# Performance work log

Measured on AMD Instinct MI355X. Metric: run time of the kernel, lower is better.

Reference implementation:

```python
import jax, jax.numpy as jnp
import numpy as np
import math

H = 1024      # hidden_size
NH = 16       # num_heads
HD = H // NH  # head_dim
MS = 256      # memory_size
MD = 512      # memory_dim
B, S = 2, 2048


def setup_inputs() -> dict:
    key = jax.random.key(0)
    ks = jax.random.split(key, 12)
    sd = 1.0 / math.sqrt(H)
    inp = {
        "hidden_states": jax.random.normal(ks[0], (B, S, H), dtype=jnp.float32),
        "attention_mask": jnp.zeros((B, S), dtype=jnp.float32),
        "Wq": jax.random.normal(ks[1], (H, H), dtype=jnp.float32) * sd,
        "bq": jnp.zeros((H,), dtype=jnp.float32),
        "Wk": jax.random.normal(ks[2], (H, H), dtype=jnp.float32) * sd,
        "bk": jnp.zeros((H,), dtype=jnp.float32),
        "Wv": jax.random.normal(ks[3], (H, H), dtype=jnp.float32) * sd,
        "bv": jnp.zeros((H,), dtype=jnp.float32),
        "Wo": jax.random.normal(ks[4], (H, H), dtype=jnp.float32) * sd,
        "bo": jnp.zeros((H,), dtype=jnp.float32),
        "memory_values": jax.random.normal(ks[5], (MS, MD), dtype=jnp.float32),
        "Wmp": jax.random.normal(ks[6], (H, MD), dtype=jnp.float32) * (1.0 / math.sqrt(MD)),
        "bmp": jnp.zeros((H,), dtype=jnp.float32),
        "Wma": jax.random.normal(ks[7], (MS, H), dtype=jnp.float32) * sd,
        "bma": jnp.zeros((MS,), dtype=jnp.float32),
    }
    return inp


def reference(hidden_states, attention_mask, Wq, bq, Wk, bk, Wv, bv, Wo, bo,
              memory_values, Wmp, bmp, Wma, bma):
    b, s, h = hidden_states.shape
    scale = math.sqrt(HD)
    # projections (nn.Linear: x @ W.T + b)
    q = hidden_states @ Wq.T + bq
    k = hidden_states @ Wk.T + bk
    v = hidden_states @ Wv.T + bv
    # [b, nh, s, hd]
    q = q.reshape(b, s, NH, HD).transpose(0, 2, 1, 3)
    k = k.reshape(b, s, NH, HD).transpose(0, 2, 1, 3)
    v = v.reshape(b, s, NH, HD).transpose(0, 2, 1, 3)
    # full score matrix [b, nh, s, s] (faithful to original naive MHA)
    attn_scores = jnp.einsum('bhqd,bhkd->bhqk', q, k) / scale
    attn_scores = attn_scores + attention_mask[:, None, None, :] * (-1e9)
    attn_probs = jax.nn.softmax(attn_scores, axis=-1)  # dropout = identity (eval)
    attn_output = jnp.einsum('bhqk,bhkd->bhqd', attn_probs, v)
    attn_output = attn_output.transpose(0, 2, 1, 3).reshape(b, s, h)
    # memory-bank cross attention
    mem_scores = hidden_states @ Wma.T + bma            # [b, s, MS]
    mem_probs = jax.nn.softmax(mem_scores, axis=-1)
    mem_out = mem_probs @ memory_values                  # [b, s, MD]
    mem_out = mem_out @ Wmp.T + bmp                      # [b, s, H]
    combined = attn_output + 0.3 * mem_out
    return combined @ Wo.T + bo
```

## Files before the change

### kernel.cpp

```cpp
#include <hip/hip_runtime.h>

typedef __bf16 bf16;
typedef __bf16 bf16x8 __attribute__((ext_vector_type(8)));
typedef __bf16 bf16x4 __attribute__((ext_vector_type(4)));
typedef float  f32x4  __attribute__((ext_vector_type(4)));
typedef float  f32x16 __attribute__((ext_vector_type(16)));
typedef unsigned u32x2 __attribute__((ext_vector_type(2)));
typedef unsigned u32x4 __attribute__((ext_vector_type(4)));
typedef unsigned long long uptr;

#define MFMA16(a, b, c) __builtin_amdgcn_mfma_f32_16x16x32_bf16((a), (b), (c), 0, 0, 0)
#define MFMA32(a, b, c) __builtin_amdgcn_mfma_f32_32x32x16_bf16((a), (b), (c), 0, 0, 0)

__device__ __forceinline__ void gl_lds16(const void* g, void* l) {
  __builtin_amdgcn_global_load_lds(
      (__attribute__((address_space(1))) void*)(uptr)(g),
      (__attribute__((address_space(3))) void*)(uptr)(l),
      16, 0, 0);
}
__device__ __forceinline__ void gl_lds4(const void* g, void* l) {
  __builtin_amdgcn_global_load_lds(
      (__attribute__((address_space(1))) void*)(uptr)(g),
      (__attribute__((address_space(3))) void*)(uptr)(l),
      4, 0, 0);
}
__device__ __forceinline__ unsigned cvtpk_bf16(float lo, float hi) {
  unsigned r;
  asm("v_cvt_pk_bf16_f32 %0, %1, %2" : "=v"(r) : "v"(lo), "v"(hi));
  return r;
}

__global__ __launch_bounds__(256) void fused_prep(
    const float* __restrict__ X, const float* __restrict__ Wq,
    const float* __restrict__ Wk, const float* __restrict__ Wv,
    const float* __restrict__ Wo, const float* __restrict__ Wma,
    const float* __restrict__ Wmp, const float* __restrict__ mask,
    const float* __restrict__ bq, const float* __restrict__ bk,
    const float* __restrict__ bv, const float* __restrict__ mv,
    bf16* __restrict__ Xb, bf16* __restrict__ Wqkvb, bf16* __restrict__ Wob,
    bf16* __restrict__ Wmab, bf16* __restrict__ Wmpb,
    float* __restrict__ M2, float* __restrict__ bqkv, bf16* __restrict__ mvTb) {
  const int bid = blockIdx.x, t = threadIdx.x;
  const float QS = 0.125f * 1.44269504f;
  auto cvt = [&](const float* src, bf16* dst, int blk, float sc) {
    const long i = ((long)blk * 256 + t) * 4;
    const float4 v = *(const float4*)(src + i);
    bf16x4 o = {(bf16)(v.x * sc), (bf16)(v.y * sc), (bf16)(v.z * sc), (bf16)(v.w * sc)};
    *(bf16x4*)(dst + i) = o;
  };
  if (bid < 4096) cvt(X, Xb, bid, 1.0f);
  else if (bid < 5120) cvt(Wq, Wqkvb, bid - 4096, QS);
  else if (bid < 6144) cvt(Wk, Wqkvb + 1024 * 1024, bid - 5120, 1.0f);
  else if (bid < 7168) cvt(Wv, Wqkvb + 2 * 1024 * 1024, bid - 6144, 1.0f);
  else if (bid < 8192) cvt(Wo, Wob, bid - 7168, 1.0f);
  else if (bid < 8448) cvt(Wma, Wmab, bid - 8192, 1.0f);
  else if (bid < 8960) cvt(Wmp, Wmpb, bid - 8448, 1.0f);
  else if (bid < 8964) {
    const long i = ((long)(bid - 8960) * 256 + t) * 4;
    const float4 v = *(const float4*)(mask + i);
    float4 o = {v.x * -1.44269504e9f - 40.0f, v.y * -1.44269504e9f - 40.0f,
                v.z * -1.44269504e9f - 40.0f, v.w * -1.44269504e9f - 40.0f};
    *(float4*)(M2 + i) = o;
  } else if (bid < 8967) {
    const int s = bid - 8964;
    const float* src = s == 0 ? bq : (s == 1 ? bk : bv);
    const float sc = s == 0 ? QS : 1.0f;
    float4 v = *(const float4*)(src + t * 4);
    float4 o = {v.x * sc, v.y * sc, v.z * sc, v.w * sc};
    *(float4*)(bqkv + s * 1024 + t * 4) = o;
  } else {
    const int d = bid - 8967;
    mvTb[(long)d * 256 + t] = (bf16)mv[(long)t * 512 + d];
  }
}

__global__ __launch_bounds__(256) void softmax_rows256(const float* __restrict__ in,
                                                       bf16* __restrict__ out) {
  const int w = threadIdx.x >> 6, l = threadIdx.x & 63;
  const long row = (long)blockIdx.x * 4 + w;
  const float4 v = *(const float4*)(in + row * 256 + l * 4);
  float mx = fmaxf(fmaxf(v.x, v.y), fmaxf(v.z, v.w));
  mx = fmaxf(mx, __shfl_xor(mx, 1, 64));
  mx = fmaxf(mx, __shfl_xor(mx, 2, 64));
  mx = fmaxf(mx, __shfl_xor(mx, 4, 64));
  mx = fmaxf(mx, __shfl_xor(mx, 8, 64));
  mx = fmaxf(mx, __shfl_xor(mx, 16, 64));
  mx = fmaxf(mx, __shfl_xor(mx, 32, 64));
  const float e0 = __expf(v.x - mx), e1 = __expf(v.y - mx);
  const float e2 = __expf(v.z - mx), e3 = __expf(v.w - mx);
  float sm = e0 + e1 + e2 + e3;
  sm += __shfl_xor(sm, 1, 64);
  sm += __shfl_xor(sm, 2, 64);
  sm += __shfl_xor(sm, 4, 64);
  sm += __shfl_xor(sm, 8, 64);
  sm += __shfl_xor(sm, 16, 64);
  sm += __shfl_xor(sm, 32, 64);
  const float inv = 1.0f / sm;
  bf16x4 o = {(bf16)(e0 * inv), (bf16)(e1 * inv), (bf16)(e2 * inv), (bf16)(e3 * inv)};
  *(bf16x4*)(out + row * 256 + l * 4) = o;
}

template <typename OutT, bool HAS_ADD>
__global__ __launch_bounds__(256, 3) void gemm_bt(
    const bf16* __restrict__ A, const bf16* __restrict__ B,
    const float* __restrict__ bias, const bf16* __restrict__ addsrc,
    OutT* __restrict__ C, int M, int N, int K, float alpha) {
  __shared__ bf16 lA[2][128 * 64];
  __shared__ bf16 lB[2][64 * 64];
  const int tid = threadIdx.x;
  const int w = tid >> 6, l = tid & 63;
  const int hi = l >> 4, lo = l & 15;
  const int m0 = blockIdx.y * 128, n0 = blockIdx.x * 64;
  const int wm = w * 32;

  const int sr8 = l >> 3;
  const int sc = (l & 7) * 8;
  const long aRow = (long)(m0 + wm + sr8);
  const long bRow = (long)(n0 + w * 16 + sr8);

  auto stage = [&](int p, int k0) {
#pragma unroll
    for (int j = 0; j < 4; ++j)
      gl_lds16(A + (aRow + 8 * j) * K + k0 + sc, (char*)lA[p] + (wm + 8 * j) * 128);
#pragma unroll
    for (int j = 0; j < 2; ++j)
      gl_lds16(B + (bRow + 8 * j) * K + k0 + sc, (char*)lB[p] + (w * 16 + 8 * j) * 128);
  };

  f32x4 acc[2][4] = {};
  stage(0, 0);
  __syncthreads();
  const int nt = K >> 6;

  for (int t = 0; t < nt; ++t) {
    const int p = t & 1;
    if (t + 1 < nt) stage(p ^ 1, (t + 1) << 6);
#pragma unroll
    for (int kk = 0; kk < 2; ++kk) {
      bf16x8 af[2], bfr[4];
#pragma unroll
      for (int mi = 0; mi < 2; ++mi)
        af[mi] = *(const bf16x8*)((const char*)lA[p] + (wm + mi * 16 + lo) * 128 + kk * 64 + hi * 16);
#pragma unroll
      for (int ni = 0; ni < 4; ++ni)
        bfr[ni] = *(const bf16x8*)((const char*)lB[p] + (ni * 16 + lo) * 128 + kk * 64 + hi * 16);
      __builtin_amdgcn_s_setprio(1);
#pragma unroll
      for (int mi = 0; mi < 2; ++mi)
#pragma unroll
        for (int ni = 0; ni < 4; ++ni)
          acc[mi][ni] = MFMA16(af[mi], bfr[ni], acc[mi][ni]);
      __builtin_amdgcn_s_setprio(0);
    }
    __syncthreads();
  }

#pragma unroll
  for (int ni = 0; ni < 4; ++ni) {
    const int col = n0 + ni * 16 + lo;
    const float bv = bias ? bias[col] : 0.0f;
#pragma unroll
    for (int mi = 0; mi < 2; ++mi) {
      const int mrow = m0 + wm + mi * 16 + hi * 4;
#pragma unroll
      for (int r = 0; r < 4; ++r) {
        const long row = mrow + r;
        float v = (acc[mi][ni][r] + bv) * alpha;
        if (HAS_ADD) v += (float)addsrc[row * N + col];
        C[row * (long)N + col] = (OutT)v;
      }
    }
  }
}

__global__ __launch_bounds__(256, 3) void gemm_qkv(
    const bf16* __restrict__ A, const bf16* __restrict__ B,
    const float* __restrict__ bias, bf16* __restrict__ Qo,
    bf16* __restrict__ Ko, bf16* __restrict__ Vto) {
  const int K = 1024;
  __shared__ bf16 smem[2][128 * 64];
  bf16* lA = smem[0];
  bf16* lB = smem[1];
  const int tid = threadIdx.x;
  const int w = tid >> 6, l = tid & 63;
  const int hi = l >> 4, lo = l & 15;
  const int m0 = blockIdx.y * 128, n0 = blockIdx.x * 128;
  const int wm = (w >> 1) * 64, wn = (w & 1) * 64;

  const int sr = w * 32 + (l >> 3);
  const int sc = (l & 7) * 8;
  const long aBase = (long)(m0 + sr) * K + sc;
  const long bBase = (long)(n0 + sr) * K + sc;

  f32x4 acc[4][4] = {};

  for (int k0 = 0; k0 < K; k0 += 64) {
#pragma unroll
    for (int j = 0; j < 4; ++j) {
      gl_lds16(A + aBase + (long)8 * j * K + k0, (char*)lA + (w * 32 + 8 * j) * 128);
      gl_lds16(B + bBase + (long)8 * j * K + k0, (char*)lB + (w * 32 + 8 * j) * 128);
    }
    __syncthreads();
#pragma unroll
    for (int kk = 0; kk < 2; ++kk) {
      bf16x8 af[4], bfr[4];
#pragma unroll
      for (int i = 0; i < 4; ++i) {
        af[i]  = *(const bf16x8*)((const char*)lA + (wm + i * 16 + lo) * 128 + kk * 64 + hi * 16);
        bfr[i] = *(const bf16x8*)((const char*)lB + (wn + i * 16 + lo) * 128 + kk * 64 + hi * 16);
      }
#pragma unroll
      for (int mi = 0; mi < 4; ++mi)
#pragma unroll
        for (int ni = 0; ni < 4; ++ni)
          acc[mi][ni] = MFMA16(af[mi], bfr[ni], acc[mi][ni]);
    }
    __syncthreads();
  }

  const int region = n0 >> 10;
  if (region < 2) {
#pragma unroll
    for (int ni = 0; ni < 4; ++ni) {
      const int col = n0 + wn + ni * 16 + lo;
      const float bv = bias[col];
#pragma unroll
      for (int mi = 0; mi < 4; ++mi) {
        const int mrow = m0 + wm + mi * 16 + hi * 4;
#pragma unroll
        for (int r = 0; r < 4; ++r) {
          const long row = mrow + r;
          const float v = acc[mi][ni][r] + bv;
          if (region == 0) Qo[row * 1024 + col] = (bf16)v;
          else             Ko[row * 1024 + (col - 1024)] = (bf16)v;
        }
      }
    }
  } else {
    bf16* sT = smem[0];
#pragma unroll
    for (int ni = 0; ni < 4; ++ni) {
      const int cT = wn + ni * 16 + lo;
      const float bv = bias[n0 + cT];
#pragma unroll
      for (int mi = 0; mi < 4; ++mi) {
        const int rT = wm + mi * 16 + hi * 4;
        u32x2 pw = {cvtpk_bf16(acc[mi][ni][0] + bv, acc[mi][ni][1] + bv),
                    cvtpk_bf16(acc[mi][ni][2] + bv, acc[mi][ni][3] + bv)};
        *(u32x2*)((char*)sT + cT * 256 + ((rT * 2) ^ ((cT & 15) << 3))) = pw;
      }
    }
    __syncthreads();
    const long vrow0 = (long)(m0 >> 11) * 1024 + (n0 - 2048);
    const int srow = m0 & 2047;
#pragma unroll
    for (int dd = 0; dd < 32; ++dd) {
      const int d = w * 32 + dd;
      const unsigned pv = *(const unsigned*)((const char*)sT + d * 256 + ((l * 4) ^ ((d & 15) << 3)));
      *(unsigned*)((char*)(Vto + (vrow0 + d) * 2048 + srow) + l * 4) = pv;
    }
  }
}

__global__ __launch_bounds__(256, 4) void attn_fwd(
    const bf16* __restrict__ Q, const bf16* __restrict__ Km,
    const bf16* __restrict__ Vt, const float* __restrict__ M2,
    bf16* __restrict__ Opart, float* __restrict__ ml) {
  __shared__ bf16 lK[2][64 * 64];
  __shared__ bf16 lV[2][64 * 64];
  __shared__ alignas(16) float lM[2][64];
  const int tid = threadIdx.x, w = tid >> 6, l = tid & 63;
  const int q31 = l & 31, h32 = l >> 5;
  const int b = blockIdx.z >> 1, half = blockIdx.z & 1;
  const int hh = blockIdx.y, q0 = blockIdx.x * 128;
  const long S = 2048, H = 1024;
  const int kbase = half * 1024;

  bf16x8 qf[4];
  const long qrow = (long)b * S + q0 + w * 32 + q31;
#pragma unroll
  for (int sl = 0; sl < 4; ++sl)
    qf[sl] = *(const bf16x8*)(Q + qrow * H + hh * 64 + sl * 16 + h32 * 8);

  f32x16 o0 = {}, o1 = {};
  float lrun = 0.0f;

  const int swr = w * 16 + (l >> 3);
  const int swc = ((l & 7) ^ (l >> 3)) * 8;

  auto stage = [&](int p, int k0) {
#pragma unroll
    for (int j = 0; j < 2; ++j) {
      gl_lds16(Km + ((long)b * S + k0 + swr + 8 * j) * H + hh * 64 + swc,
               (char*)lK[p] + (w * 16 + 8 * j) * 128);
      gl_lds16(Vt + ((long)b * H + hh * 64 + swr + 8 * j) * S + k0 + swc,
               (char*)lV[p] + (w * 16 + 8 * j) * 128);
    }
    if (w == 0) gl_lds4(M2 + (long)b * S + k0 + l, (char*)lM[p]);
  };

  stage(0, kbase);
  __syncthreads();

  for (int t = 0; t < 16; ++t) {
    const int p = t & 1;
    if (t < 15) stage(p ^ 1, kbase + (t + 1) * 64);

    f32x16 s0, s1;
#pragma unroll
    for (int g = 0; g < 4; ++g) {
      const f32x4 m0 = *(const f32x4*)&lM[p][8 * g + 4 * h32];
      const f32x4 m1 = *(const f32x4*)&lM[p][32 + 8 * g + 4 * h32];
#pragma unroll
      for (int r = 0; r < 4; ++r) {
        s0[4 * g + r] = m0[r];
        s1[4 * g + r] = m1[r];
      }
    }

    __builtin_amdgcn_s_setprio(1);
#pragma unroll
    for (int sl = 0; sl < 4; ++sl) {
      const int ch = sl * 2 + h32;
      const int cx = (ch ^ (q31 & 7)) * 16;
      const bf16x8 k0f = *(const bf16x8*)((const char*)lK[p] + q31 * 128 + cx);
      const bf16x8 k1f = *(const bf16x8*)((const char*)lK[p] + (32 + q31) * 128 + cx);
      s0 = MFMA32(k0f, qf[sl], s0);
      s1 = MFMA32(k1f, qf[sl], s1);
    }
    __builtin_amdgcn_s_setprio(0);

#pragma unroll
    for (int i = 0; i < 16; ++i) s0[i] = __builtin_amdgcn_exp2f(s0[i]);
#pragma unroll
    for (int i = 0; i < 16; ++i) s1[i] = __builtin_amdgcn_exp2f(s1[i]);

    f32x16 ts;
#pragma unroll
    for (int i = 0; i < 16; ++i) ts[i] = s0[i] + s1[i];
#pragma unroll
    for (int i = 0; i < 8; ++i) ts[i] += ts[i + 8];
#pragma unroll
    for (int i = 0; i < 4; ++i) ts[i] += ts[i + 4];
    float rs = (ts[0] + ts[1]) + (ts[2] + ts[3]);
    rs += __shfl_xor(rs, 32, 64);
    lrun += rs;

    bf16x8 pa[4];
#pragma unroll
    for (int ks = 0; ks < 4; ++ks) {
      const int rb = (ks & 1) * 8;
      unsigned a0, a1, b0, b1;
      if (ks < 2) {
        a0 = cvtpk_bf16(s0[rb + 0], s0[rb + 1]);
        a1 = cvtpk_bf16(s0[rb + 2], s0[rb + 3]);
        b0 = cvtpk_bf16(s0[rb + 4], s0[rb + 5]);
        b1 = cvtpk_bf16(s0[rb + 6], s0[rb + 7]);
      } else {
        a0 = cvtpk_bf16(s1[rb + 0], s1[rb + 1]);
        a1 = cvtpk_bf16(s1[rb + 2], s1[rb + 3]);
        b0 = cvtpk_bf16(s1[rb + 4], s1[rb + 5]);
        b1 = cvtpk_bf16(s1[rb + 6], s1[rb + 7]);
      }
      const u32x2 r02 = __builtin_amdgcn_permlane32_swap(a0, b0, false, false);
      const u32x2 r13 = __builtin_amdgcn_permlane32_swap(a1, b1, false, false);
      const u32x4 pw = {r02[0], r13[0], r02[1], r13[1]};
      pa[ks] = __builtin_bit_cast(bf16x8, pw);
    }

    __builtin_amdgcn_s_setprio(1);
#pragma unroll
    for (int ks = 0; ks < 4; ++ks) {
      const int ch = ks * 2 + h32;
      const int cx = (ch ^ (q31 & 7)) * 16;
      const bf16x8 v0 = *(const bf16x8*)((const char*)lV[p] + q31 * 128 + cx);
      const bf16x8 v1 = *(const bf16x8*)((const char*)lV[p] + (32 + q31) * 128 + cx);
      o0 = MFMA32(pa[ks], v0, o0);
      o1 = MFMA32(pa[ks], v1, o1);
    }
    __builtin_amdgcn_s_setprio(0);
    __syncthreads();
  }

  if (h32 == 0)
    ml[((long)half * 4096 + (long)b * 2048 + q0 + w * 32 + q31) * 16 + hh] = lrun;
#pragma unroll
  for (int reg = 0; reg < 16; ++reg) {
    const int row = (reg & 3) + 8 * (reg >> 2) + 4 * h32;
    const long qg = (long)b * 2048 + q0 + w * 32 + row;
    Opart[((long)half * 4096 + qg) * 1024 + hh * 64 + q31]      = (bf16)o0[reg];
    Opart[((long)half * 4096 + qg) * 1024 + hh * 64 + 32 + q31] = (bf16)o1[reg];
  }
}

__global__ __launch_bounds__(256) void attn_combine(
    const bf16* __restrict__ Opart, const float* __restrict__ ml,
    bf16* __restrict__ AO) {
  const long i = ((long)blockIdx.x * 256 + threadIdx.x) * 4;
  const long qg = i >> 10;
  const int h = (int)((i & 1023) >> 6);
  const float l0 = ml[qg * 16 + h];
  const float l1 = ml[(4096 + qg) * 16 + h];
  const float inv = 1.0f / (l0 + l1);
  const bf16x4 O0 = *(const bf16x4*)(Opart + i);
  const bf16x4 O1 = *(const bf16x4*)(Opart + 4096L * 1024 + i);
  bf16x4 o;
#pragma unroll
  for (int j = 0; j < 4; ++j)
    o[j] = (bf16)(((float)O0[j] + (float)O1[j]) * inv);
  *(bf16x4*)(AO + i) = o;
}

extern "C" void kernel_launch(void* const* d_in, const int* in_sizes, int n_in,
                              void* d_out, int out_size, void* d_ws, size_t ws_size,
                              hipStream_t stream) {
  const float* X    = (const float*)d_in[0];
  const float* mask = (const float*)d_in[1];
  const float* Wq   = (const float*)d_in[2];  const float* bq  = (const float*)d_in[3];
  const float* Wk   = (const float*)d_in[4];  const float* bk  = (const float*)d_in[5];
  const float* Wv   = (const float*)d_in[6];  const float* bv  = (const float*)d_in[7];
  const float* Wo   = (const float*)d_in[8];  const float* bo  = (const float*)d_in[9];
  const float* mv   = (const float*)d_in[10];
  const float* Wmp  = (const float*)d_in[11]; const float* bmp = (const float*)d_in[12];
  const float* Wma  = (const float*)d_in[13]; const float* bma = (const float*)d_in[14];

  char* ws = (char*)d_ws;
  size_t off = 0;
  auto alloc = [&](size_t bytes) -> void* {
    void* p = ws + off;
    off += (bytes + 255) & ~(size_t)255;
    return p;
  };
  const long MS_ = 4096;
  bf16* Xb    = (bf16*)alloc(MS_ * 1024 * 2);
  bf16* Wqkvb = (bf16*)alloc(3072L * 1024 * 2);
  bf16* Wob   = (bf16*)alloc(1024 * 1024 * 2);
  bf16* Wmab  = (bf16*)alloc(256 * 1024 * 2);
  bf16* Wmpb  = (bf16*)alloc(1024 * 512 * 2);
  bf16* mvTb  = (bf16*)alloc(512 * 256 * 2);
  float* M2   = (float*)alloc(MS_ * 4);
  float* bqkv = (float*)alloc(3072 * 4);
  bf16* Qb    = (bf16*)alloc(MS_ * 1024 * 2);
  bf16* Kb    = (bf16*)alloc(MS_ * 1024 * 2);
  bf16* Vtb   = (bf16*)alloc(MS_ * 1024 * 2);
  bf16* AO    = (bf16*)alloc(MS_ * 1024 * 2);
  char* region = (char*)alloc(2 * MS_ * 1024 * 2 + MS_ * 16 * 8 + 1024);
  bf16* Opart = (bf16*)region;
  float* ml   = (float*)(region + 2 * MS_ * 1024 * 2);
  float* MSc  = (float*)region;
  bf16* MP    = (bf16*)(region + MS_ * 256 * 4);
  bf16* MO    = Kb;
  bf16* CB    = Qb;

  fused_prep<<<9479, 256, 0, stream>>>(X, Wq, Wk, Wv, Wo, Wma, Wmp, mask,
                                       bq, bk, bv, mv,
                                       Xb, Wqkvb, Wob, Wmab, Wmpb, M2, bqkv, mvTb);
  gemm_qkv<<<dim3(24, 32), 256, 0, stream>>>(Xb, Wqkvb, bqkv, Qb, Kb, Vtb);
  attn_fwd<<<dim3(16, 16, 4), 256, 0, stream>>>(Qb, Kb, Vtb, M2, Opart, ml);
  attn_combine<<<4096, 256, 0, stream>>>(Opart, ml, AO);
  gemm_bt<float, false><<<dim3(4, 32), 256, 0, stream>>>(Xb, Wmab, bma, nullptr, MSc, 4096, 256, 1024, 1.0f);
  softmax_rows256<<<1024, 256, 0, stream>>>(MSc, MP);
  gemm_bt<bf16, false><<<dim3(8, 32), 256, 0, stream>>>(MP, mvTb, nullptr, nullptr, MO, 4096, 512, 256, 1.0f);
  gemm_bt<bf16, true><<<dim3(16, 32), 256, 0, stream>>>(MO, Wmpb, bmp, AO, CB, 4096, 1024, 512, 0.3f);
  gemm_bt<float, false><<<dim3(16, 32), 256, 0, stream>>>(CB, Wob, bo, nullptr, (float*)d_out, 4096, 1024, 1024, 1.0f);
}
```

Measured before the change: 148.4 us.

## Fuse memory-score GEMM into QKV GEMM and attention combine into Wmp epilogue

Appends the Wma weights and bias to the concatenated QKV weight matrix, so the QKV GEMM grid grows by two column tiles and also writes the fp32 memory scores. This removes the separate memory-score GEMM launch. It also drops the attn_combine kernel and merges the two split-K attention partials inside the Wmp GEMM epilogue, which removes an extra pass over the AO buffer. The trade-off is a heavier epilogue with scattered ml/Opart loads and a per-element divide, plus separate workspace buffers instead of aliased ones.

```diff
diff --git a/kernel.cpp b/kernel.cpp
--- a/kernel.cpp
+++ b/kernel.cpp
@@ -36,9 +36,10 @@
     const float* __restrict__ Wo, const float* __restrict__ Wma,
     const float* __restrict__ Wmp, const float* __restrict__ mask,
     const float* __restrict__ bq, const float* __restrict__ bk,
-    const float* __restrict__ bv, const float* __restrict__ mv,
+    const float* __restrict__ bv, const float* __restrict__ bma,
+    const float* __restrict__ mv,
     bf16* __restrict__ Xb, bf16* __restrict__ Wqkvb, bf16* __restrict__ Wob,
-    bf16* __restrict__ Wmab, bf16* __restrict__ Wmpb,
+    bf16* __restrict__ Wmpb,
     float* __restrict__ M2, float* __restrict__ bqkv, bf16* __restrict__ mvTb) {
   const int bid = blockIdx.x, t = threadIdx.x;
   const float QS = 0.125f * 1.44269504f;
@@ -53,7 +54,7 @@
   else if (bid < 6144) cvt(Wk, Wqkvb + 1024 * 1024, bid - 5120, 1.0f);
   else if (bid < 7168) cvt(Wv, Wqkvb + 2 * 1024 * 1024, bid - 6144, 1.0f);
   else if (bid < 8192) cvt(Wo, Wob, bid - 7168, 1.0f);
-  else if (bid < 8448) cvt(Wma, Wmab, bid - 8192, 1.0f);
+  else if (bid < 8448) cvt(Wma, Wqkvb + 3072 * 1024, bid - 8192, 1.0f);
   else if (bid < 8960) cvt(Wmp, Wmpb, bid - 8448, 1.0f);
   else if (bid < 8964) {
     const long i = ((long)(bid - 8960) * 256 + t) * 4;
@@ -68,8 +69,10 @@
     float4 v = *(const float4*)(src + t * 4);
     float4 o = {v.x * sc, v.y * sc, v.z * sc, v.w * sc};
     *(float4*)(bqkv + s * 1024 + t * 4) = o;
+  } else if (bid < 8968) {
+    if (t < 64) *(float4*)(bqkv + 3072 + t * 4) = *(const float4*)(bma + t * 4);
   } else {
-    const int d = bid - 8967;
+    const int d = bid - 8968;
     mvTb[(long)d * 256 + t] = (bf16)mv[(long)t * 512 + d];
   }
 }
@@ -100,11 +103,12 @@
   *(bf16x4*)(out + row * 256 + l * 4) = o;
 }
 
-template <typename OutT, bool HAS_ADD>
+template <typename OutT, bool COMBINE>
 __global__ __launch_bounds__(256, 3) void gemm_bt(
     const bf16* __restrict__ A, const bf16* __restrict__ B,
-    const float* __restrict__ bias, const bf16* __restrict__ addsrc,
-    OutT* __restrict__ C, int M, int N, int K, float alpha) {
+    const float* __restrict__ bias, const bf16* __restrict__ Op,
+    const float* __restrict__ mlp, OutT* __restrict__ C,
+    int M, int N, int K, float alpha) {
   __shared__ bf16 lA[2][128 * 64];
   __shared__ bf16 lB[2][64 * 64];
   const int tid = threadIdx.x;
@@ -166,7 +170,14 @@
       for (int r = 0; r < 4; ++r) {
         const long row = mrow + r;
         float v = (acc[mi][ni][r] + bv) * alpha;
-        if (HAS_ADD) v += (float)addsrc[row * N + col];
+        if (COMBINE) {
+          const int h = col >> 6;
+          const float l0 = mlp[row * 16 + h];
+          const float l1 = mlp[(4096L + row) * 16 + h];
+          const float o0v = (float)Op[row * 1024 + col];
+          const float o1v = (float)Op[4096L * 1024 + row * 1024 + col];
+          v += (o0v + o1v) / (l0 + l1);
+        }
         C[row * (long)N + col] = (OutT)v;
       }
     }
@@ -176,7 +187,7 @@
 __global__ __launch_bounds__(256, 3) void gemm_qkv(
     const bf16* __restrict__ A, const bf16* __restrict__ B,
     const float* __restrict__ bias, bf16* __restrict__ Qo,
-    bf16* __restrict__ Ko, bf16* __restrict__ Vto) {
+    bf16* __restrict__ Ko, bf16* __restrict__ Vto, float* __restrict__ MSc) {
   const int K = 1024;
   __shared__ bf16 smem[2][128 * 64];
   bf16* lA = smem[0];
@@ -218,8 +229,7 @@
     __syncthreads();
   }
 
-  const int region = n0 >> 10;
-  if (region < 2) {
+  if (n0 < 2048) {
 #pragma unroll
     for (int ni = 0; ni < 4; ++ni) {
       const int col = n0 + wn + ni * 16 + lo;
@@ -231,12 +241,12 @@
         for (int r = 0; r < 4; ++r) {
           const long row = mrow + r;
           const float v = acc[mi][ni][r] + bv;
-          if (region == 0) Qo[row * 1024 + col] = (bf16)v;
-          else             Ko[row * 1024 + (col - 1024)] = (bf16)v;
+          if (n0 < 1024) Qo[row * 1024 + col] = (bf16)v;
+          else           Ko[row * 1024 + (col - 1024)] = (bf16)v;
         }
       }
     }
-  } else {
+  } else if (n0 < 3072) {
     bf16* sT = smem[0];
 #pragma unroll
     for (int ni = 0; ni < 4; ++ni) {
@@ -258,6 +268,20 @@
       const int d = w * 32 + dd;
       const unsigned pv = *(const unsigned*)((const char*)sT + d * 256 + ((l * 4) ^ ((d & 15) << 3)));
       *(unsigned*)((char*)(Vto + (vrow0 + d) * 2048 + srow) + l * 4) = pv;
+    }
+  } else {
+#pragma unroll
+    for (int ni = 0; ni < 4; ++ni) {
+      const int col = n0 + wn + ni * 16 + lo;
+      const float bv = bias[col];
+      const int cm = col - 3072;
+#pragma unroll
+      for (int mi = 0; mi < 4; ++mi) {
+        const int mrow = m0 + wm + mi * 16 + hi * 4;
+#pragma unroll
+        for (int r = 0; r < 4; ++r)
+          MSc[(long)(mrow + r) * 256 + cm] = acc[mi][ni][r] + bv;
+      }
     }
   }
 }
@@ -393,24 +417,6 @@
   }
 }
 
-__global__ __launch_bounds__(256) void attn_combine(
-    const bf16* __restrict__ Opart, const float* __restrict__ ml,
-    bf16* __restrict__ AO) {
-  const long i = ((long)blockIdx.x * 256 + threadIdx.x) * 4;
-  const long qg = i >> 10;
-  const int h = (int)((i & 1023) >> 6);
-  const float l0 = ml[qg * 16 + h];
-  const float l1 = ml[(4096 + qg) * 16 + h];
-  const float inv = 1.0f / (l0 + l1);
-  const bf16x4 O0 = *(const bf16x4*)(Opart + i);
-  const bf16x4 O1 = *(const bf16x4*)(Opart + 4096L * 1024 + i);
-  bf16x4 o;
-#pragma unroll
-  for (int j = 0; j < 4; ++j)
-    o[j] = (bf16)(((float)O0[j] + (float)O1[j]) * inv);
-  *(bf16x4*)(AO + i) = o;
-}
-
 extern "C" void kernel_launch(void* const* d_in, const int* in_sizes, int n_in,
                               void* d_out, int out_size, void* d_ws, size_t ws_size,
                               hipStream_t stream) {
@@ -433,34 +439,32 @@
   };
   const long MS_ = 4096;
   bf16* Xb    = (bf16*)alloc(MS_ * 1024 * 2);
-  bf16* Wqkvb = (bf16*)alloc(3072L * 1024 * 2);
+  bf16* Wqkvb = (bf16*)alloc(3328L * 1024 * 2);
   bf16* Wob   = (bf16*)alloc(1024 * 1024 * 2);
-  bf16* Wmab  = (bf16*)alloc(256 * 1024 * 2);
   bf16* Wmpb  = (bf16*)alloc(1024 * 512 * 2);
   bf16* mvTb  = (bf16*)alloc(512 * 256 * 2);
   float* M2   = (float*)alloc(MS_ * 4);
-  float* bqkv = (float*)alloc(3072 * 4);
+  float* bqkv = (float*)alloc(3328 * 4);
   bf16* Qb    = (bf16*)alloc(MS_ * 1024 * 2);
   bf16* Kb    = (bf16*)alloc(MS_ * 1024 * 2);
   bf16* Vtb   = (bf16*)alloc(MS_ * 1024 * 2);
-  bf16* AO    = (bf16*)alloc(MS_ * 1024 * 2);
-  char* region = (char*)alloc(2 * MS_ * 1024 * 2 + MS_ * 16 * 8 + 1024);
-  bf16* Opart = (bf16*)region;
-  float* ml   = (float*)(region + 2 * MS_ * 1024 * 2);
-  float* MSc  = (float*)region;
-  bf16* MP    = (bf16*)(region + MS_ * 256 * 4);
+  bf16* Opart = (bf16*)alloc(2 * MS_ * 1024 * 2);
+  float* ml   = (float*)alloc(2 * MS_ * 16 * 4);
+  float* MSc  = (float*)alloc(MS_ * 256 * 4);
+  bf16* MP    = (bf16*)alloc(MS_ * 256 * 2);
   bf16* MO    = Kb;
   bf16* CB    = Qb;
 
-  fused_prep<<<9479, 256, 0, stream>>>(X, Wq, Wk, Wv, Wo, Wma, Wmp, mask,
-                                       bq, bk, bv, mv,
-                                       Xb, Wqkvb, Wob, Wmab, Wmpb, M2, bqkv, mvTb);
-  gemm_qkv<<<dim3(24, 32), 256, 0, stream>>>(Xb, Wqkvb, bqkv, Qb, Kb, Vtb);
+  fused_prep<<<9480, 256, 0, stream>>>(X, Wq, Wk, Wv, Wo, Wma, Wmp, mask,
+                                       bq, bk, bv, bma, mv,
+                                       Xb, Wqkvb, Wob, Wmpb, M2, bqkv, mvTb);
+  gemm_qkv<<<dim3(26, 32), 256, 0, stream>>>(Xb, Wqkvb, bqkv, Qb, Kb, Vtb, MSc);
   attn_fwd<<<dim3(16, 16, 4), 256, 0, stream>>>(Qb, Kb, Vtb, M2, Opart, ml);
-  attn_combine<<<4096, 256, 0, stream>>>(Opart, ml, AO);
-  gemm_bt<float, false><<<dim3(4, 32), 256, 0, stream>>>(Xb, Wmab, bma, nullptr, MSc, 4096, 256, 1024, 1.0f);
   softmax_rows256<<<1024, 256, 0, stream>>>(MSc, MP);
-  gemm_bt<bf16, false><<<dim3(8, 32), 256, 0, stream>>>(MP, mvTb, nullptr, nullptr, MO, 4096, 512, 256, 1.0f);
-  gemm_bt<bf16, true><<<dim3(16, 32), 256, 0, stream>>>(MO, Wmpb, bmp, AO, CB, 4096, 1024, 512, 0.3f);
-  gemm_bt<float, false><<<dim3(16, 32), 256, 0, stream>>>(CB, Wob, bo, nullptr, (float*)d_out, 4096, 1024, 1024, 1.0f);
-}
+  gemm_bt<bf16, false><<<dim3(8, 32), 256, 0, stream>>>(MP, mvTb, nullptr, nullptr, nullptr,
+                                                        MO, 4096, 512, 256, 1.0f);
+  gemm_bt<bf16, true><<<dim3(16, 32), 256, 0, stream>>>(MO, Wmpb, bmp, Opart, ml,
+                                                        CB, 4096, 1024, 512, 0.3f);
+  gemm_bt<float, false><<<dim3(16, 32), 256, 0, stream>>>(CB, Wob, bo, nullptr, nullptr,
+                                                          (float*)d_out, 4096, 1024, 1024, 1.0f);
+}
```

New measurement: 140.0 us. -5.7%, faster.
